# Kernel optimization log

Measured on AMD Instinct MI355X. Metric: run time of the kernel, lower is better.

The kernel has to match this reference:

```python
import jax, jax.numpy as jnp
import numpy as np


def setup_inputs() -> dict:
    key = jax.random.key(0)
    k1, k2 = jax.random.split(key)
    shape = (4096, 16384)  # d_model x d_ff weight matrix, 64M elements
    weight = jax.random.normal(k1, shape, dtype=jnp.float32)
    mask_weights = jax.random.normal(k2, shape, dtype=jnp.float32)
    return {"weight": weight, "mask_weights": mask_weights, "masking_percent": 0.5}


def reference(weight, mask_weights, masking_percent):
    # torch: topk(mask_weights.flat, k=int((1-p)*N), largest=False) -> zero those
    # positions in a clone of weight.
    flat_mask = mask_weights.reshape(-1)
    n = flat_mask.shape[0]
    k = int((1.0 - masking_percent) * n)  # static python int (p is a python float)
    # bottom-k of mask_weights == top-k of its negation
    _, bottomk_idx = jax.lax.top_k(-flat_mask, k)
    masked = weight.reshape(-1).at[bottomk_idx].set(0.0)
    return masked.reshape(weight.shape)
```

## Files before the change

kernel.cpp:

```cpp
#include <hip/hip_runtime.h>

#define HIST_BITS 12
#define NBINS (1 << HIST_BITS)
#define KEY_SHIFT (32 - HIST_BITS)
#define REP 4

typedef float fx4 __attribute__((ext_vector_type(4)));

struct Ctrl {
    long long k;
    long long r1;
    int b1;
    unsigned counter;
};

__device__ __forceinline__ unsigned fkey(float f) {
    unsigned u = __float_as_uint(f);
    return (u & 0x80000000u) ? ~u : (u | 0x80000000u);
}

__global__ void k_zero(unsigned* __restrict__ hist, Ctrl* __restrict__ ctrl) {
    int i = blockIdx.x * blockDim.x + threadIdx.x;
    if (i < NBINS) hist[i] = 0;
    if (i == 0) {
        ctrl->k = 0;
        ctrl->r1 = 0;
        ctrl->b1 = -1;
        ctrl->counter = 0;
    }
}

__global__ void __launch_bounds__(256)
k_hist(const float* __restrict__ mask, long long n, unsigned* __restrict__ ghist) {
    __shared__ unsigned sh[NBINS * REP];
    for (int i = threadIdx.x; i < NBINS * REP; i += blockDim.x) sh[i] = 0;
    __syncthreads();

    const unsigned r = threadIdx.x & (REP - 1);
    const long long n4 = n >> 2;
    const fx4* m4 = (const fx4*)mask;
    const long long S = (long long)gridDim.x * blockDim.x;
    long long i = (long long)blockIdx.x * blockDim.x + threadIdx.x;

    for (; i + 3 * S < n4; i += 4 * S) {
        fx4 a = m4[i];
        fx4 b = m4[i + S];
        fx4 c = m4[i + 2 * S];
        fx4 d = m4[i + 3 * S];
        atomicAdd(&sh[(fkey(a.x) >> KEY_SHIFT) * REP + r], 1u);
        atomicAdd(&sh[(fkey(a.y) >> KEY_SHIFT) * REP + r], 1u);
        atomicAdd(&sh[(fkey(a.z) >> KEY_SHIFT) * REP + r], 1u);
        atomicAdd(&sh[(fkey(a.w) >> KEY_SHIFT) * REP + r], 1u);
        atomicAdd(&sh[(fkey(b.x) >> KEY_SHIFT) * REP + r], 1u);
        atomicAdd(&sh[(fkey(b.y) >> KEY_SHIFT) * REP + r], 1u);
        atomicAdd(&sh[(fkey(b.z) >> KEY_SHIFT) * REP + r], 1u);
        atomicAdd(&sh[(fkey(b.w) >> KEY_SHIFT) * REP + r], 1u);
        atomicAdd(&sh[(fkey(c.x) >> KEY_SHIFT) * REP + r], 1u);
        atomicAdd(&sh[(fkey(c.y) >> KEY_SHIFT) * REP + r], 1u);
        atomicAdd(&sh[(fkey(c.z) >> KEY_SHIFT) * REP + r], 1u);
        atomicAdd(&sh[(fkey(c.w) >> KEY_SHIFT) * REP + r], 1u);
        atomicAdd(&sh[(fkey(d.x) >> KEY_SHIFT) * REP + r], 1u);
        atomicAdd(&sh[(fkey(d.y) >> KEY_SHIFT) * REP + r], 1u);
        atomicAdd(&sh[(fkey(d.z) >> KEY_SHIFT) * REP + r], 1u);
        atomicAdd(&sh[(fkey(d.w) >> KEY_SHIFT) * REP + r], 1u);
    }
    for (; i < n4; i += S) {
        fx4 a = m4[i];
        atomicAdd(&sh[(fkey(a.x) >> KEY_SHIFT) * REP + r], 1u);
        atomicAdd(&sh[(fkey(a.y) >> KEY_SHIFT) * REP + r], 1u);
        atomicAdd(&sh[(fkey(a.z) >> KEY_SHIFT) * REP + r], 1u);
        atomicAdd(&sh[(fkey(a.w) >> KEY_SHIFT) * REP + r], 1u);
    }
    if (blockIdx.x == 0 && threadIdx.x == 0) {
        for (long long t = n4 * 4; t < n; ++t)
            atomicAdd(&ghist[fkey(mask[t]) >> KEY_SHIFT], 1u);
    }
    __syncthreads();
    for (int b = threadIdx.x; b < NBINS; b += blockDim.x) {
        unsigned s = sh[b * REP] + sh[b * REP + 1] + sh[b * REP + 2] + sh[b * REP + 3];
        if (s) atomicAdd(&ghist[b], s);
    }
}

__global__ void k_scan(const unsigned* __restrict__ ghist, Ctrl* __restrict__ ctrl,
                       const float* __restrict__ p_ptr, long long n) {
    __shared__ long long part[256];
    __shared__ long long kk_sh;
    const int t = threadIdx.x;
    if (t == 0) {
        double p = (double)p_ptr[0];
        long long k = (long long)((1.0 - p) * (double)n);
        if (k < 0) k = 0;
        if (k > n) k = n;
        kk_sh = k;
        ctrl->k = k;
        ctrl->b1 = -1;
        ctrl->r1 = 0;
    }
    __syncthreads();
    const long long k = kk_sh;

    const int per = NBINS / 256;
    long long s = 0;
    for (int i = 0; i < per; ++i) s += (long long)ghist[t * per + i];
    part[t] = s;
    __syncthreads();
    for (int off = 1; off < 256; off <<= 1) {
        long long add = (t >= off) ? part[t - off] : 0;
        __syncthreads();
        part[t] += add;
        __syncthreads();
    }
    if (k >= 1) {
        long long incl = part[t];
        long long excl = incl - s;
        if (excl < k && k <= incl) {
            long long cum = excl;
            for (int i = 0; i < per; ++i) {
                long long c = (long long)ghist[t * per + i];
                if (cum < k && k <= cum + c) {
                    ctrl->b1 = t * per + i;
                    ctrl->r1 = k - cum;
                    break;
                }
                cum += c;
            }
        }
    }
}

__device__ __forceinline__ float apply1(float m, float w, unsigned idx, int b1,
                                        Ctrl* ctrl, uint2* list, unsigned cap) {
    unsigned key = fkey(m);
    int bin = (int)(key >> KEY_SHIFT);
    if (bin < b1) return 0.0f;
    if (bin == b1) {
        unsigned pos = atomicAdd(&ctrl->counter, 1u);
        if (pos < cap) list[pos] = make_uint2(key, idx);
    }
    return w;
}

__global__ void __launch_bounds__(256)
k_apply(const float* __restrict__ w, const float* __restrict__ mask,
        float* __restrict__ out, long long n,
        Ctrl* __restrict__ ctrl, uint2* __restrict__ list, unsigned cap) {
    const int b1 = ctrl->b1;
    const long long n4 = n >> 2;
    const fx4* m4 = (const fx4*)mask;
    const fx4* w4 = (const fx4*)w;
    fx4* o4 = (fx4*)out;
    const long long S = (long long)gridDim.x * blockDim.x;
    long long i = (long long)blockIdx.x * blockDim.x + threadIdx.x;

    for (; i + S < n4; i += 2 * S) {
        fx4 m0 = m4[i];
        fx4 m1 = m4[i + S];
        fx4 w0 = __builtin_nontemporal_load(&w4[i]);
        fx4 w1 = __builtin_nontemporal_load(&w4[i + S]);
        fx4 o0, o1;
        unsigned base0 = (unsigned)(i * 4);
        unsigned base1 = (unsigned)((i + S) * 4);
        o0.x = apply1(m0.x, w0.x, base0 + 0, b1, ctrl, list, cap);
        o0.y = apply1(m0.y, w0.y, base0 + 1, b1, ctrl, list, cap);
        o0.z = apply1(m0.z, w0.z, base0 + 2, b1, ctrl, list, cap);
        o0.w = apply1(m0.w, w0.w, base0 + 3, b1, ctrl, list, cap);
        o1.x = apply1(m1.x, w1.x, base1 + 0, b1, ctrl, list, cap);
        o1.y = apply1(m1.y, w1.y, base1 + 1, b1, ctrl, list, cap);
        o1.z = apply1(m1.z, w1.z, base1 + 2, b1, ctrl, list, cap);
        o1.w = apply1(m1.w, w1.w, base1 + 3, b1, ctrl, list, cap);
        __builtin_nontemporal_store(o0, &o4[i]);
        __builtin_nontemporal_store(o1, &o4[i + S]);
    }
    for (; i < n4; i += S) {
        fx4 m0 = m4[i];
        fx4 w0 = __builtin_nontemporal_load(&w4[i]);
        fx4 o0;
        unsigned base0 = (unsigned)(i * 4);
        o0.x = apply1(m0.x, w0.x, base0 + 0, b1, ctrl, list, cap);
        o0.y = apply1(m0.y, w0.y, base0 + 1, b1, ctrl, list, cap);
        o0.z = apply1(m0.z, w0.z, base0 + 2, b1, ctrl, list, cap);
        o0.w = apply1(m0.w, w0.w, base0 + 3, b1, ctrl, list, cap);
        __builtin_nontemporal_store(o0, &o4[i]);
    }
    if (blockIdx.x == 0 && threadIdx.x == 0) {
        for (long long t = n4 * 4; t < n; ++t)
            out[t] = apply1(mask[t], w[t], (unsigned)t, b1, ctrl, list, cap);
    }
}

__global__ void k_fix(float* __restrict__ out, const Ctrl* __restrict__ ctrl,
                      const uint2* __restrict__ list, unsigned cap) {
    __shared__ uint2 ch[1024];
    unsigned nc = ctrl->counter;
    if (nc > cap) nc = cap;
    const long long r1 = ctrl->r1;
    if (ctrl->b1 < 0 || r1 <= 0) return;

    for (unsigned jb = 0; jb < nc; jb += blockDim.x) {
        unsigned j = jb + threadIdx.x;
        bool act = (j < nc);
        unsigned kj = 0, ij = 0;
        if (act) { uint2 e = list[j]; kj = e.x; ij = e.y; }
        long long rank = 0;
        for (unsigned cb = 0; cb < nc; cb += 1024) {
            unsigned mlen = nc - cb; if (mlen > 1024) mlen = 1024;
            for (unsigned u = threadIdx.x; u < mlen; u += blockDim.x) ch[u] = list[cb + u];
            __syncthreads();
            if (act) {
                for (unsigned u = 0; u < mlen; ++u) {
                    uint2 e = ch[u];
                    rank += (long long)((e.x < kj) || (e.x == kj && e.y < ij));
                }
            }
            __syncthreads();
        }
        if (act && rank < r1) out[ij] = 0.0f;
    }
}

extern "C" void kernel_launch(void* const* d_in, const int* in_sizes, int n_in,
                              void* d_out, int out_size, void* d_ws, size_t ws_size,
                              hipStream_t stream) {
    const float* weight = (const float*)d_in[0];
    const float* maskw  = (const float*)d_in[1];
    const float* pptr   = (const float*)d_in[2];
    float* out = (float*)d_out;
    const long long n = (long long)in_sizes[0];

    unsigned char* ws = (unsigned char*)d_ws;
    unsigned* hist = (unsigned*)ws;
    Ctrl* ctrl = (Ctrl*)(ws + 16384);
    uint2* list = (uint2*)(ws + 16416);
    size_t cap_sz = (ws_size > 16416) ? (ws_size - 16416) / sizeof(uint2) : 0;
    unsigned cap = (unsigned)(cap_sz > (size_t)(1u << 20) ? (1u << 20) : cap_sz);

    k_zero<<<(NBINS + 255) / 256, 256, 0, stream>>>(hist, ctrl);
    k_hist<<<2048, 256, 0, stream>>>(maskw, n, hist);
    k_scan<<<1, 256, 0, stream>>>(hist, ctrl, pptr, n);
    k_apply<<<2048, 256, 0, stream>>>(weight, maskw, out, n, ctrl, list, cap);
    k_fix<<<1, 256, 0, stream>>>(out, ctrl, list, cap);
}
```

Measured before the change: 215.5 us.

## Split apply into bitmap-building mask pass and bitmap-driven weight apply

Adds a kernel that reads the mask once, records boundary-bin candidates and writes a per-element keep bitmap via wave ballots. A second kernel then reads only the weights plus that compact bitmap to produce the output. The aim is to stop the weight-apply pass from streaming the full mask. The cost is an extra launch and an extra full pass over the mask, so total traffic is about the same. The original fused path is kept as a fallback when the workspace is too small.

```diff
diff --git a/kernel.cpp b/kernel.cpp
--- a/kernel.cpp
+++ b/kernel.cpp
@@ -6,6 +6,7 @@
 #define REP 4
 
 typedef float fx4 __attribute__((ext_vector_type(4)));
+typedef unsigned long long ull;
 
 struct Ctrl {
     long long k;
@@ -23,10 +24,7 @@
     int i = blockIdx.x * blockDim.x + threadIdx.x;
     if (i < NBINS) hist[i] = 0;
     if (i == 0) {
-        ctrl->k = 0;
-        ctrl->r1 = 0;
-        ctrl->b1 = -1;
-        ctrl->counter = 0;
+        ctrl->k = 0; ctrl->r1 = 0; ctrl->b1 = -1; ctrl->counter = 0;
     }
 }
 
@@ -129,6 +127,114 @@
     }
 }
 
+__global__ void __launch_bounds__(256)
+k_bm(const float* __restrict__ mask, long long n, Ctrl* __restrict__ ctrl,
+     ull* __restrict__ bm, uint2* __restrict__ list, unsigned cap) {
+    const int b1 = ctrl->b1;
+    const long long n4 = n >> 2;
+    const long long chunks = (n4 + 63) >> 6;
+    const fx4* m4 = (const fx4*)mask;
+    const int lane = threadIdx.x & 63;
+    const long long wid = (long long)blockIdx.x * (blockDim.x >> 6) + (threadIdx.x >> 6);
+    const long long nw = (long long)gridDim.x * (blockDim.x >> 6);
+
+    for (long long ch = wid; ch < chunks; ch += nw) {
+        long long g = ch * 64 + lane;
+        bool valid = g < n4;
+        fx4 m;
+        if (valid) m = m4[g]; else { m.x = m.y = m.z = m.w = 0.0f; }
+        unsigned kx = fkey(m.x), ky = fkey(m.y), kz = fkey(m.z), kw = fkey(m.w);
+        int bx = (int)(kx >> KEY_SHIFT), by = (int)(ky >> KEY_SHIFT);
+        int bz = (int)(kz >> KEY_SHIFT), bw = (int)(kw >> KEY_SHIFT);
+        if (valid) {
+            unsigned base = (unsigned)(g * 4);
+            if (bx == b1) { unsigned p = atomicAdd(&ctrl->counter, 1u); if (p < cap) list[p] = make_uint2(kx, base + 0); }
+            if (by == b1) { unsigned p = atomicAdd(&ctrl->counter, 1u); if (p < cap) list[p] = make_uint2(ky, base + 1); }
+            if (bz == b1) { unsigned p = atomicAdd(&ctrl->counter, 1u); if (p < cap) list[p] = make_uint2(kz, base + 2); }
+            if (bw == b1) { unsigned p = atomicAdd(&ctrl->counter, 1u); if (p < cap) list[p] = make_uint2(kw, base + 3); }
+        }
+        ull w0 = __ballot(bx >= b1);
+        ull w1 = __ballot(by >= b1);
+        ull w2 = __ballot(bz >= b1);
+        ull w3 = __ballot(bw >= b1);
+        if (lane < 4) {
+            ull w = (lane == 0) ? w0 : (lane == 1) ? w1 : (lane == 2) ? w2 : w3;
+            bm[ch * 4 + lane] = w;
+        }
+    }
+    if (blockIdx.x == 0 && threadIdx.x == 0) {
+        for (long long t = n4 * 4; t < n; ++t) {
+            unsigned key = fkey(mask[t]);
+            if ((int)(key >> KEY_SHIFT) == b1) {
+                unsigned p = atomicAdd(&ctrl->counter, 1u);
+                if (p < cap) list[p] = make_uint2(key, (unsigned)t);
+            }
+        }
+    }
+}
+
+__global__ void __launch_bounds__(256)
+k_apply_bm(const float* __restrict__ w, const ull* __restrict__ bm,
+           const float* __restrict__ mask, float* __restrict__ out, long long n,
+           const Ctrl* __restrict__ ctrl) {
+    const long long n4 = n >> 2;
+    const long long chunks = (n4 + 63) >> 6;
+    const fx4* w4 = (const fx4*)w;
+    fx4* o4 = (fx4*)out;
+    const int lane = threadIdx.x & 63;
+    const ull lm = 1ull << lane;
+    const long long wid = (long long)blockIdx.x * (blockDim.x >> 6) + (threadIdx.x >> 6);
+    const long long nw = (long long)gridDim.x * (blockDim.x >> 6);
+
+    long long ch = wid;
+    for (; ch + nw < chunks; ch += 2 * nw) {
+        long long g0 = ch * 64 + lane;
+        long long g1 = (ch + nw) * 64 + lane;
+        fx4 wa, wb;
+        if (g0 < n4) wa = __builtin_nontemporal_load(&w4[g0]);
+        if (g1 < n4) wb = __builtin_nontemporal_load(&w4[g1]);
+        ull a0 = bm[ch * 4 + 0], a1 = bm[ch * 4 + 1], a2 = bm[ch * 4 + 2], a3 = bm[ch * 4 + 3];
+        ull b0 = bm[(ch + nw) * 4 + 0], b1v = bm[(ch + nw) * 4 + 1];
+        ull b2 = bm[(ch + nw) * 4 + 2], b3 = bm[(ch + nw) * 4 + 3];
+        if (g0 < n4) {
+            fx4 o;
+            o.x = (a0 & lm) ? wa.x : 0.0f;
+            o.y = (a1 & lm) ? wa.y : 0.0f;
+            o.z = (a2 & lm) ? wa.z : 0.0f;
+            o.w = (a3 & lm) ? wa.w : 0.0f;
+            __builtin_nontemporal_store(o, &o4[g0]);
+        }
+        if (g1 < n4) {
+            fx4 o;
+            o.x = (b0 & lm) ? wb.x : 0.0f;
+            o.y = (b1v & lm) ? wb.y : 0.0f;
+            o.z = (b2 & lm) ? wb.z : 0.0f;
+            o.w = (b3 & lm) ? wb.w : 0.0f;
+            __builtin_nontemporal_store(o, &o4[g1]);
+        }
+    }
+    for (; ch < chunks; ch += nw) {
+        long long g = ch * 64 + lane;
+        if (g < n4) {
+            fx4 wv = __builtin_nontemporal_load(&w4[g]);
+            ull a0 = bm[ch * 4 + 0], a1 = bm[ch * 4 + 1], a2 = bm[ch * 4 + 2], a3 = bm[ch * 4 + 3];
+            fx4 o;
+            o.x = (a0 & lm) ? wv.x : 0.0f;
+            o.y = (a1 & lm) ? wv.y : 0.0f;
+            o.z = (a2 & lm) ? wv.z : 0.0f;
+            o.w = (a3 & lm) ? wv.w : 0.0f;
+            __builtin_nontemporal_store(o, &o4[g]);
+        }
+    }
+    if (blockIdx.x == 0 && threadIdx.x == 0) {
+        const int b1 = ctrl->b1;
+        for (long long t = n4 * 4; t < n; ++t) {
+            int bin = (int)(fkey(mask[t]) >> KEY_SHIFT);
+            out[t] = (bin < b1) ? 0.0f : w[t];
+        }
+    }
+}
+
 __device__ __forceinline__ float apply1(float m, float w, unsigned idx, int b1,
                                         Ctrl* ctrl, uint2* list, unsigned cap) {
     unsigned key = fkey(m);
@@ -142,9 +248,9 @@
 }
 
 __global__ void __launch_bounds__(256)
-k_apply(const float* __restrict__ w, const float* __restrict__ mask,
-        float* __restrict__ out, long long n,
-        Ctrl* __restrict__ ctrl, uint2* __restrict__ list, unsigned cap) {
+k_apply_mask(const float* __restrict__ w, const float* __restrict__ mask,
+             float* __restrict__ out, long long n,
+             Ctrl* __restrict__ ctrl, uint2* __restrict__ list, unsigned cap) {
     const int b1 = ctrl->b1;
     const long long n4 = n >> 2;
     const fx4* m4 = (const fx4*)mask;
@@ -152,26 +258,6 @@
     fx4* o4 = (fx4*)out;
     const long long S = (long long)gridDim.x * blockDim.x;
     long long i = (long long)blockIdx.x * blockDim.x + threadIdx.x;
-
-    for (; i + S < n4; i += 2 * S) {
-        fx4 m0 = m4[i];
-        fx4 m1 = m4[i + S];
-        fx4 w0 = __builtin_nontemporal_load(&w4[i]);
-        fx4 w1 = __builtin_nontemporal_load(&w4[i + S]);
-        fx4 o0, o1;
-        unsigned base0 = (unsigned)(i * 4);
-        unsigned base1 = (unsigned)((i + S) * 4);
-        o0.x = apply1(m0.x, w0.x, base0 + 0, b1, ctrl, list, cap);
-        o0.y = apply1(m0.y, w0.y, base0 + 1, b1, ctrl, list, cap);
-        o0.z = apply1(m0.z, w0.z, base0 + 2, b1, ctrl, list, cap);
-        o0.w = apply1(m0.w, w0.w, base0 + 3, b1, ctrl, list, cap);
-        o1.x = apply1(m1.x, w1.x, base1 + 0, b1, ctrl, list, cap);
-        o1.y = apply1(m1.y, w1.y, base1 + 1, b1, ctrl, list, cap);
-        o1.z = apply1(m1.z, w1.z, base1 + 2, b1, ctrl, list, cap);
-        o1.w = apply1(m1.w, w1.w, base1 + 3, b1, ctrl, list, cap);
-        __builtin_nontemporal_store(o0, &o4[i]);
-        __builtin_nontemporal_store(o1, &o4[i + S]);
-    }
     for (; i < n4; i += S) {
         fx4 m0 = m4[i];
         fx4 w0 = __builtin_nontemporal_load(&w4[i]);
@@ -232,12 +318,25 @@
     unsigned* hist = (unsigned*)ws;
     Ctrl* ctrl = (Ctrl*)(ws + 16384);
     uint2* list = (uint2*)(ws + 16416);
-    size_t cap_sz = (ws_size > 16416) ? (ws_size - 16416) / sizeof(uint2) : 0;
-    unsigned cap = (unsigned)(cap_sz > (size_t)(1u << 20) ? (1u << 20) : cap_sz);
+    const size_t BM_OFF = (size_t)16 << 20;
+    unsigned cap = (unsigned)((BM_OFF - 16416) / sizeof(uint2));
+
+    const long long n4 = n >> 2;
+    const long long chunks = (n4 + 63) >> 6;
+    const size_t bm_bytes = (size_t)chunks * 4 * sizeof(ull);
+    const bool use_bm = ws_size >= BM_OFF + bm_bytes + 64;
+    ull* bm = (ull*)(ws + BM_OFF);
 
     k_zero<<<(NBINS + 255) / 256, 256, 0, stream>>>(hist, ctrl);
     k_hist<<<2048, 256, 0, stream>>>(maskw, n, hist);
     k_scan<<<1, 256, 0, stream>>>(hist, ctrl, pptr, n);
-    k_apply<<<2048, 256, 0, stream>>>(weight, maskw, out, n, ctrl, list, cap);
+    if (use_bm) {
+        k_bm<<<2048, 256, 0, stream>>>(maskw, n, ctrl, bm, list, cap);
+        k_apply_bm<<<2048, 256, 0, stream>>>(weight, bm, maskw, out, n, ctrl);
+    } else {
+        size_t cap_sz = (ws_size > 16416) ? (ws_size - 16416) / sizeof(uint2) : 0;
+        unsigned cap2 = (unsigned)(cap_sz > (size_t)(1u << 20) ? (1u << 20) : cap_sz);
+        k_apply_mask<<<2048, 256, 0, stream>>>(weight, maskw, out, n, ctrl, list, cap2);
+    }
     k_fix<<<1, 256, 0, stream>>>(out, ctrl, list, cap);
 }
```

Measured after the change: 231.5 us. 7.4% more time.
